# Kernel tuning notes

Hardware: AMD Instinct MI355X
Metric: run time of the kernel (lower is better)

## Reference

```python
import jax, jax.numpy as jnp
import numpy as np
import math

FACTOR = 1

def setup_inputs() -> dict:
    key = jax.random.key(0)
    k1, k2, k3 = jax.random.split(key, 3)
    B, L, V, H, E = 4, 96, 207, 8, 64
    return {
        "queries": jax.random.normal(k1, (B, L, V, H, E), dtype=jnp.float32),
        "keys": jax.random.normal(k2, (B, L, V, H, E), dtype=jnp.float32),
        "values": jax.random.normal(k3, (B, L, V, H, E), dtype=jnp.float32),
    }

def reference(queries, keys, values):
    B, L, V, H, E = queries.shape
    # L == S here; torch code truncates keys/values to length L
    keys = keys[:, :L]
    values = values[:, :L]
    # [B,L,V,H,E] -> [B,H,E,V,L]
    q = jnp.transpose(queries, (0, 3, 4, 2, 1))
    k = jnp.transpose(keys, (0, 3, 4, 2, 1))
    v = jnp.transpose(values, (0, 3, 4, 2, 1))
    # period-based dependency discovery via FFT cross-correlation
    q_fft = jnp.fft.rfft(q, axis=-1)
    k_fft = jnp.fft.rfft(k, axis=-1)
    corr = jnp.fft.irfft(q_fft * jnp.conj(k_fft), n=L, axis=-1)  # [B,H,E,V,L]

    top_k = int(FACTOR * math.log(L))  # static: L is a trace-time constant
    mean_value = corr.mean(axis=1).mean(axis=1)  # [B,V,L]
    # training branch: indices from batch-mean correlation
    global_mean = mean_value.mean(axis=0)  # [V,L]
    _, index = jax.lax.top_k(global_mean, top_k)  # [V,K]
    weights = jnp.take_along_axis(
        mean_value, jnp.broadcast_to(index[None], (B, V, top_k)), axis=-1
    )  # [B,V,K]
    tmp_corr = jax.nn.softmax(weights, axis=-1)  # [B,V,K]

    # time-delay aggregation: weighted sum of per-vertex rolled values.
    # Loop over small fixed top_k (=4) to avoid the [B,H,E,V,L,K] blowup.
    l_idx = jnp.arange(L)
    agg = jnp.zeros_like(v)
    for kk in range(top_k):
        idxmat = (l_idx[None, :] + index[:, kk:kk + 1]) % L  # [V,L]
        rolled = jnp.take_along_axis(v, idxmat[None, None, None], axis=-1)  # [B,H,E,V,L]
        agg = agg + rolled * tmp_corr[:, None, None, :, kk:kk + 1]
    # [B,H,E,V,L] -> [B,L,V,E,H] (matches torch permute(0,4,3,2,1))
    return jnp.transpose(agg, (0, 4, 3, 2, 1))
```

## Files before the change

### kernel.cpp

```cpp
#include <hip/hip_runtime.h>

#define B 4
#define L 96
#define V 207
#define H 8
#define E 64
#define C 512
#define LS (V*C)
#define TOPK 4
#define LPAD 68
#define TPAD 132

#define MV_OFF 0
#define IDX_OFF (B*V*L*4)
#define TC_OFF  (IDX_OFF + V*TOPK*4)

__global__ __launch_bounds__(256) void corr_mean_kernel(
        const float* __restrict__ q, const float* __restrict__ k,
        float* __restrict__ mv) {
    __shared__ float Qs[L * LPAD];
    __shared__ float Ks[L * LPAD];
    __shared__ float corr[L];

    const int bid = blockIdx.x;
    const int b = bid / V;
    const int v = bid % V;
    const int tid = threadIdx.x;
    const int ti = tid >> 4;
    const int tj = tid & 15;

    const size_t base = ((size_t)b * L * V + v) * (size_t)C;

    float acc[6][6];
#pragma unroll
    for (int i = 0; i < 6; i++)
#pragma unroll
        for (int j = 0; j < 6; j++) acc[i][j] = 0.f;

    for (int c0 = 0; c0 < C; c0 += 64) {
#pragma unroll
        for (int it = 0; it < 6; it++) {
            const int id = tid + it * 256;
            const int t = id >> 4;
            const int fc = (id & 15) << 2;
            const size_t g = base + (size_t)t * LS + c0 + fc;
            const float4 qv = *(const float4*)(q + g);
            const float4 kv = *(const float4*)(k + g);
            *(float4*)(Qs + t * LPAD + fc) = qv;
            *(float4*)(Ks + t * LPAD + fc) = kv;
        }
        __syncthreads();

#pragma unroll 4
        for (int cc = 0; cc < 64; cc++) {
            float qr[6], kr[6];
#pragma unroll
            for (int i = 0; i < 6; i++) qr[i] = Qs[(ti + 16 * i) * LPAD + cc];
#pragma unroll
            for (int j = 0; j < 6; j++) kr[j] = Ks[(tj + 16 * j) * LPAD + cc];
#pragma unroll
            for (int i = 0; i < 6; i++)
#pragma unroll
                for (int j = 0; j < 6; j++)
                    acc[i][j] = fmaf(qr[i], kr[j], acc[i][j]);
        }
        __syncthreads();
    }

    if (tid < L) corr[tid] = 0.f;
    __syncthreads();

#pragma unroll
    for (int d = -5; d <= 5; d++) {
        float s = 0.f;
#pragma unroll
        for (int i = 0; i < 6; i++) {
            const int j = i - d;
            if (j >= 0 && j < 6) s += acc[i][j];
        }
        int tau = ti - tj + 16 * d;
        tau = ((tau % L) + L) % L;
        atomicAdd(&corr[tau], s);
    }
    __syncthreads();

    if (tid < L) mv[((size_t)b * V + v) * L + tid] = corr[tid] * (1.0f / 512.0f);
}

__global__ __launch_bounds__(128) void topk_softmax_kernel(
        const float* __restrict__ mv, int* __restrict__ idx,
        float* __restrict__ tc) {
    __shared__ float gm[L];
    __shared__ int sidx[TOPK];
    const int v = blockIdx.x;
    const int tid = threadIdx.x;

    if (tid < L) {
        float s = 0.f;
        for (int b = 0; b < B; b++) s += mv[((size_t)b * V + v) * L + tid];
        gm[tid] = s;
    }
    __syncthreads();

    if (tid == 0) {
        for (int kk = 0; kk < TOPK; kk++) {
            float best = -1e30f;
            int bi = 0;
            for (int t = 0; t < L; t++)
                if (gm[t] > best) { best = gm[t]; bi = t; }
            sidx[kk] = bi;
            gm[bi] = -1e30f;
        }
        for (int kk = 0; kk < TOPK; kk++) idx[v * TOPK + kk] = sidx[kk];
    }
    __syncthreads();

    if (tid < B) {
        const int b = tid;
        float w[TOPK];
        float m = -1e30f;
        for (int kk = 0; kk < TOPK; kk++) {
            w[kk] = mv[((size_t)b * V + v) * L + sidx[kk]];
            m = fmaxf(m, w[kk]);
        }
        float s = 0.f;
        for (int kk = 0; kk < TOPK; kk++) { w[kk] = expf(w[kk] - m); s += w[kk]; }
        const float inv = 1.f / s;
        for (int kk = 0; kk < TOPK; kk++)
            tc[((size_t)b * V + v) * TOPK + kk] = w[kk] * inv;
    }
}

__global__ __launch_bounds__(256) void agg_kernel(
        const float* __restrict__ val, const float* __restrict__ tc,
        const int* __restrict__ idx, float* __restrict__ out) {
    __shared__ __attribute__((aligned(16))) float T[L * TPAD];
    __shared__ int sidx[TOPK];
    __shared__ float sw[TOPK];

    const int bid = blockIdx.x;
    const int qtr = bid & 3;
    const int bv = bid >> 2;
    const int b = bv / V;
    const int v = bv % V;
    const int tid = threadIdx.x;
    const int e0 = qtr * 16;

    const size_t base = ((size_t)b * L * V + v) * (size_t)C;

    if (tid < TOPK) {
        sidx[tid] = idx[v * TOPK + tid];
        sw[tid] = tc[((size_t)b * V + v) * TOPK + tid];
    }

#pragma unroll
    for (int it = 0; it < 12; it++) {
        const int id = tid + it * 256;
        const int l = id >> 5;
        const int h = (id & 31) >> 2;
        const int f4 = id & 3;
        const float4 r = *(const float4*)(val + base + (size_t)l * LS + h * 64 + e0 + f4 * 4);
        float* dst = T + l * TPAD + f4 * 32 + h;
        dst[0]  = r.x;
        dst[8]  = r.y;
        dst[16] = r.z;
        dst[24] = r.w;
    }
    __syncthreads();

    const float w0 = sw[0], w1 = sw[1], w2 = sw[2], w3 = sw[3];
    const int i0 = sidx[0], i1 = sidx[1], i2 = sidx[2], i3 = sidx[3];

#pragma unroll
    for (int it = 0; it < 12; it++) {
        const int id = tid + it * 256;
        const int l = id >> 5;
        const int m = id & 31;
        int l0 = l + i0; if (l0 >= L) l0 -= L;
        int l1 = l + i1; if (l1 >= L) l1 -= L;
        int l2 = l + i2; if (l2 >= L) l2 -= L;
        int l3 = l + i3; if (l3 >= L) l3 -= L;
        const float4 r0 = *(const float4*)(T + l0 * TPAD + m * 4);
        const float4 r1 = *(const float4*)(T + l1 * TPAD + m * 4);
        const float4 r2 = *(const float4*)(T + l2 * TPAD + m * 4);
        const float4 r3 = *(const float4*)(T + l3 * TPAD + m * 4);
        float4 o;
        o.x = w0 * r0.x + w1 * r1.x + w2 * r2.x + w3 * r3.x;
        o.y = w0 * r0.y + w1 * r1.y + w2 * r2.y + w3 * r3.y;
        o.z = w0 * r0.z + w1 * r1.z + w2 * r2.z + w3 * r3.z;
        o.w = w0 * r0.w + w1 * r1.w + w2 * r2.w + w3 * r3.w;
        *(float4*)(out + base + (size_t)l * LS + qtr * 128 + m * 4) = o;
    }
}

extern "C" void kernel_launch(void* const* d_in, const int* in_sizes, int n_in,
                              void* d_out, int out_size, void* d_ws, size_t ws_size,
                              hipStream_t stream) {
    const float* q = (const float*)d_in[0];
    const float* k = (const float*)d_in[1];
    const float* val = (const float*)d_in[2];
    float* out = (float*)d_out;
    char* ws = (char*)d_ws;
    float* mv = (float*)(ws + MV_OFF);
    int* idx = (int*)(ws + IDX_OFF);
    float* tc = (float*)(ws + TC_OFF);

    corr_mean_kernel<<<B * V, 256, 0, stream>>>(q, k, mv);
    topk_softmax_kernel<<<V, 128, 0, stream>>>(mv, idx, tc);
    agg_kernel<<<B * V * 4, 256, 0, stream>>>(val, tc, idx, out);
}
```

Measured before the change: 555.3 us.

## Use split-fp16 MFMA for correlation, wave-parallel top-k, swizzled agg LDS

```diff
diff --git a/kernel.cpp b/kernel.cpp
--- a/kernel.cpp
+++ b/kernel.cpp
@@ -8,61 +8,101 @@
 #define C 512
 #define LS (V*C)
 #define TOPK 4
-#define LPAD 68
-#define TPAD 132
+#define QPAD 68
+#define TPAD 128
 
 #define MV_OFF 0
 #define IDX_OFF (B*V*L*4)
 #define TC_OFF  (IDX_OFF + V*TOPK*4)
 
+typedef float f32x4 __attribute__((ext_vector_type(4)));
+typedef _Float16 f16x8 __attribute__((ext_vector_type(8)));
+
 __global__ __launch_bounds__(256) void corr_mean_kernel(
         const float* __restrict__ q, const float* __restrict__ k,
         float* __restrict__ mv) {
-    __shared__ float Qs[L * LPAD];
-    __shared__ float Ks[L * LPAD];
+    __shared__ __attribute__((aligned(16))) float Qs[L * QPAD];
+    __shared__ __attribute__((aligned(16))) float Ks[L * QPAD];
     __shared__ float corr[L];
 
     const int bid = blockIdx.x;
     const int b = bid / V;
     const int v = bid % V;
     const int tid = threadIdx.x;
-    const int ti = tid >> 4;
-    const int tj = tid & 15;
+    const int lane = tid & 63;
+    const int wave = tid >> 6;
+    const int lrow = lane & 15;
+    const int lq = lane >> 4;
+    const int rbase = (wave >> 1) * 48;
+    const int cbase = (wave & 1) * 48;
 
     const size_t base = ((size_t)b * L * V + v) * (size_t)C;
 
-    float acc[6][6];
-#pragma unroll
-    for (int i = 0; i < 6; i++)
-#pragma unroll
-        for (int j = 0; j < 6; j++) acc[i][j] = 0.f;
+    f32x4 acc[3][3];
+#pragma unroll
+    for (int i = 0; i < 3; i++)
+#pragma unroll
+        for (int j = 0; j < 3; j++) acc[i][j] = (f32x4){0.f, 0.f, 0.f, 0.f};
 
     for (int c0 = 0; c0 < C; c0 += 64) {
 #pragma unroll
         for (int it = 0; it < 6; it++) {
             const int id = tid + it * 256;
             const int t = id >> 4;
-            const int fc = (id & 15) << 2;
-            const size_t g = base + (size_t)t * LS + c0 + fc;
+            const int s = id & 15;
+            const size_t g = base + (size_t)t * LS + c0 + s * 4;
             const float4 qv = *(const float4*)(q + g);
             const float4 kv = *(const float4*)(k + g);
-            *(float4*)(Qs + t * LPAD + fc) = qv;
-            *(float4*)(Ks + t * LPAD + fc) = kv;
+            *(float4*)(Qs + t * QPAD + s * 4) = qv;
+            *(float4*)(Ks + t * QPAD + s * 4) = kv;
         }
         __syncthreads();
 
-#pragma unroll 4
-        for (int cc = 0; cc < 64; cc++) {
-            float qr[6], kr[6];
-#pragma unroll
-            for (int i = 0; i < 6; i++) qr[i] = Qs[(ti + 16 * i) * LPAD + cc];
-#pragma unroll
-            for (int j = 0; j < 6; j++) kr[j] = Ks[(tj + 16 * j) * LPAD + cc];
-#pragma unroll
-            for (int i = 0; i < 6; i++)
-#pragma unroll
-                for (int j = 0; j < 6; j++)
-                    acc[i][j] = fmaf(qr[i], kr[j], acc[i][j]);
+#pragma unroll
+        for (int kk = 0; kk < 2; kk++) {
+            const int soff = kk * 32 + lq * 8;
+            f16x8 qh[3], ql[3], kh[3], kl[3];
+#pragma unroll
+            for (int ti = 0; ti < 3; ti++) {
+                const int t = rbase + ti * 16 + lrow;
+                const float* p = Qs + t * QPAD + soff;
+                const float4 a0 = *(const float4*)(p);
+                const float4 a1 = *(const float4*)(p + 4);
+                const float xs[8] = {a0.x, a0.y, a0.z, a0.w,
+                                     a1.x, a1.y, a1.z, a1.w};
+#pragma unroll
+                for (int j = 0; j < 8; j++) {
+                    const _Float16 h = (_Float16)xs[j];
+                    qh[ti][j] = h;
+                    ql[ti][j] = (_Float16)(xs[j] - (float)h);
+                }
+            }
+#pragma unroll
+            for (int tj = 0; tj < 3; tj++) {
+                const int t = cbase + tj * 16 + lrow;
+                const float* p = Ks + t * QPAD + soff;
+                const float4 a0 = *(const float4*)(p);
+                const float4 a1 = *(const float4*)(p + 4);
+                const float xs[8] = {a0.x, a0.y, a0.z, a0.w,
+                                     a1.x, a1.y, a1.z, a1.w};
+#pragma unroll
+                for (int j = 0; j < 8; j++) {
+                    const _Float16 h = (_Float16)xs[j];
+                    kh[tj][j] = h;
+                    kl[tj][j] = (_Float16)(xs[j] - (float)h);
+                }
+            }
+#pragma unroll
+            for (int ti = 0; ti < 3; ti++)
+#pragma unroll
+                for (int tj = 0; tj < 3; tj++) {
+                    acc[ti][tj] = __builtin_amdgcn_mfma_f32_16x16x32_f16(
+                        qh[ti], kh[tj], acc[ti][tj], 0, 0, 0);
+                    acc[ti][tj] = __builtin_amdgcn_mfma_f32_16x16x32_f16(
+                        qh[ti], kl[tj], acc[ti][tj], 0, 0, 0);
+                    acc[ti][tj] = __builtin_amdgcn_mfma_f32_16x16x32_f16(
+                        ql[ti], kh[tj], acc[ti][tj], 0, 0, 0);
+                }
         }
         __syncthreads();
     }
@@ -71,23 +111,26 @@
     __syncthreads();
 
 #pragma unroll
-    for (int d = -5; d <= 5; d++) {
-        float s = 0.f;
-#pragma unroll
-        for (int i = 0; i < 6; i++) {
-            const int j = i - d;
-            if (j >= 0 && j < 6) s += acc[i][j];
-        }
-        int tau = ti - tj + 16 * d;
-        tau = ((tau % L) + L) % L;
-        atomicAdd(&corr[tau], s);
+    for (int d = -2; d <= 2; d++) {
+        f32x4 s = (f32x4){0.f, 0.f, 0.f, 0.f};
+#pragma unroll
+        for (int ti = 0; ti < 3; ti++) {
+            const int tj = ti - d;
+            if (tj >= 0 && tj < 3) s += acc[ti][tj];
+        }
+#pragma unroll
+        for (int r = 0; r < 4; r++) {
+            int tau = rbase - cbase + d * 16 + lq * 4 + r - lrow;
+            tau = ((tau % L) + L) % L;
+            atomicAdd(&corr[tau], s[r]);
+        }
     }
     __syncthreads();
 
     if (tid < L) mv[((size_t)b * V + v) * L + tid] = corr[tid] * (1.0f / 512.0f);
 }
 
-__global__ __launch_bounds__(128) void topk_softmax_kernel(
+__global__ __launch_bounds__(64) void topk_softmax_kernel(
         const float* __restrict__ mv, int* __restrict__ idx,
         float* __restrict__ tc) {
     __shared__ float gm[L];
@@ -95,40 +138,53 @@
     const int v = blockIdx.x;
     const int tid = threadIdx.x;
 
-    if (tid < L) {
-        float s = 0.f;
-        for (int b = 0; b < B; b++) s += mv[((size_t)b * V + v) * L + tid];
-        gm[tid] = s;
-    }
-    __syncthreads();
-
-    if (tid == 0) {
-        for (int kk = 0; kk < TOPK; kk++) {
-            float best = -1e30f;
-            int bi = 0;
-            for (int t = 0; t < L; t++)
-                if (gm[t] > best) { best = gm[t]; bi = t; }
-            sidx[kk] = bi;
-            gm[bi] = -1e30f;
-        }
-        for (int kk = 0; kk < TOPK; kk++) idx[v * TOPK + kk] = sidx[kk];
-    }
-    __syncthreads();
+    {
+        float s0 = 0.f, s1 = 0.f;
+#pragma unroll
+        for (int b = 0; b < B; b++) {
+            s0 += mv[((size_t)b * V + v) * L + tid];
+            if (tid < 32) s1 += mv[((size_t)b * V + v) * L + 64 + tid];
+        }
+        gm[tid] = s0;
+        if (tid < 32) gm[64 + tid] = s1;
+    }
+    __syncthreads();
+
+    for (int kk = 0; kk < TOPK; kk++) {
+        float val = gm[tid];
+        int id2 = tid;
+        if (tid < 32) {
+            const float v2 = gm[64 + tid];
+            if (v2 > val) { val = v2; id2 = 64 + tid; }
+        }
+#pragma unroll
+        for (int off = 32; off > 0; off >>= 1) {
+            const float ov = __shfl_xor(val, off);
+            const int oi = __shfl_xor(id2, off);
+            if (ov > val || (ov == val && oi < id2)) { val = ov; id2 = oi; }
+        }
+        if (tid == 0) { sidx[kk] = id2; gm[id2] = -1e30f; }
+        __syncthreads();
+    }
 
     if (tid < B) {
         const int b = tid;
         float w[TOPK];
         float m = -1e30f;
+#pragma unroll
         for (int kk = 0; kk < TOPK; kk++) {
             w[kk] = mv[((size_t)b * V + v) * L + sidx[kk]];
             m = fmaxf(m, w[kk]);
         }
         float s = 0.f;
+#pragma unroll
         for (int kk = 0; kk < TOPK; kk++) { w[kk] = expf(w[kk] - m); s += w[kk]; }
         const float inv = 1.f / s;
+#pragma unroll
         for (int kk = 0; kk < TOPK; kk++)
             tc[((size_t)b * V + v) * TOPK + kk] = w[kk] * inv;
     }
+    if (tid < TOPK) idx[v * TOPK + tid] = sidx[tid];
 }
 
 __global__ __launch_bounds__(256) void agg_kernel(
@@ -138,7 +194,8 @@
     __shared__ int sidx[TOPK];
     __shared__ float sw[TOPK];
 
-    const int bid = blockIdx.x;
+    const int p = blockIdx.x;
+    const int bid = (p & 7) * ((B * V * 4) / 8) + (p >> 3);
     const int qtr = bid & 3;
     const int bv = bid >> 2;
     const int b = bv / V;
@@ -161,10 +218,10 @@
         const int f4 = id & 3;
         const float4 r = *(const float4*)(val + base + (size_t)l * LS + h * 64 + e0 + f4 * 4);
         float* dst = T + l * TPAD + f4 * 32 + h;
-        dst[0]  = r.x;
-        dst[8]  = r.y;
-        dst[16] = r.z;
-        dst[24] = r.w;
+        dst[(0 ^ f4) * 8] = r.x;
+        dst[(1 ^ f4) * 8] = r.y;
+        dst[(2 ^ f4) * 8] = r.z;
+        dst[(3 ^ f4) * 8] = r.w;
     }
     __syncthreads();
 
@@ -176,14 +233,17 @@
         const int id = tid + it * 256;
         const int l = id >> 5;
         const int m = id & 31;
+        const int f4 = m >> 3;
+        const int w = m & 7;
+        const int off = f4 * 32 + (((((w >> 1) ^ f4) << 1) | (w & 1)) << 2);
         int l0 = l + i0; if (l0 >= L) l0 -= L;
         int l1 = l + i1; if (l1 >= L) l1 -= L;
         int l2 = l + i2; if (l2 >= L) l2 -= L;
         int l3 = l + i3; if (l3 >= L) l3 -= L;
-        const float4 r0 = *(const float4*)(T + l0 * TPAD + m * 4);
-        const float4 r1 = *(const float4*)(T + l1 * TPAD + m * 4);
-        const float4 r2 = *(const float4*)(T + l2 * TPAD + m * 4);
-        const float4 r3 = *(const float4*)(T + l3 * TPAD + m * 4);
+        const float4 r0 = *(const float4*)(T + l0 * TPAD + off);
+        const float4 r1 = *(const float4*)(T + l1 * TPAD + off);
+        const float4 r2 = *(const float4*)(T + l2 * TPAD + off);
+        const float4 r3 = *(const float4*)(T + l3 * TPAD + off);
         float4 o;
         o.x = w0 * r0.x + w1 * r1.x + w2 * r2.x + w3 * r3.x;
         o.y = w0 * r0.y + w1 * r1.y + w2 * r2.y + w3 * r3.y;
@@ -206,6 +266,6 @@
     float* tc = (float*)(ws + TC_OFF);
 
     corr_mean_kernel<<<B * V, 256, 0, stream>>>(q, k, mv);
-    topk_softmax_kernel<<<V, 128, 0, stream>>>(mv, idx, tc);
+    topk_softmax_kernel<<<V, 64, 0, stream>>>(mv, idx, tc);
     agg_kernel<<<B * V * 4, 256, 0, stream>>>(val, tc, idx, out);
 }
```

After: 502.1 us. 1.11x faster.
